# Performance work log

Hardware: AMD Instinct MI355X
Metric: run time of the kernel (lower is better)

## Reference

```python
import jax, jax.numpy as jnp
import numpy as np

HIDDEN = 512
HEADS = 8
HEAD_DIM = HIDDEN // HEADS
MAX_DIST = 10
B, N = 16, 512
EPS = 1e-5


def _layer_norm(x, g, b):
    mu = jnp.mean(x, axis=-1, keepdims=True)
    var = jnp.mean(jnp.square(x - mu), axis=-1, keepdims=True)
    return (x - mu) * jax.lax.rsqrt(var + EPS) * g + b


def setup_inputs() -> dict:
    key = jax.random.key(0)
    ks = jax.random.split(key, 16)
    s = 0.02
    inp = {
        "x": jax.random.normal(ks[0], (B, N, HIDDEN), jnp.float32),
        "distances": jax.random.randint(ks[1], (B, N, N), 0, MAX_DIST, jnp.int32),
        "edge_features": jax.random.normal(ks[2], (B, N, N), jnp.float32),
        "attn_mask": jax.random.randint(ks[3], (B, N), 0, 2).astype(bool),
        "Wq": jax.random.normal(ks[4], (HIDDEN, HIDDEN), jnp.float32) * s,
        "bq": jnp.zeros((HIDDEN,), jnp.float32),
        "Wk": jax.random.normal(ks[5], (HIDDEN, HIDDEN), jnp.float32) * s,
        "bk": jnp.zeros((HIDDEN,), jnp.float32),
        "Wv": jax.random.normal(ks[6], (HIDDEN, HIDDEN), jnp.float32) * s,
        "bv": jnp.zeros((HIDDEN,), jnp.float32),
        "Wo": jax.random.normal(ks[7], (HIDDEN, HIDDEN), jnp.float32) * s,
        "bo": jnp.zeros((HIDDEN,), jnp.float32),
        "spatial_emb": jax.random.normal(ks[8], (MAX_DIST, HEADS), jnp.float32) * s,
        "edge_w": jax.random.normal(ks[9], (HEADS,), jnp.float32) * s,
        "edge_b": jnp.zeros((HEADS,), jnp.float32),
        "ln1_g": jnp.ones((HIDDEN,), jnp.float32),
        "ln1_b": jnp.zeros((HIDDEN,), jnp.float32),
        "ln2_g": jnp.ones((HIDDEN,), jnp.float32),
        "ln2_b": jnp.zeros((HIDDEN,), jnp.float32),
        "W1": jax.random.normal(ks[10], (HIDDEN, 4 * HIDDEN), jnp.float32) * s,
        "b1": jnp.zeros((4 * HIDDEN,), jnp.float32),
        "W2": jax.random.normal(ks[11], (4 * HIDDEN, HIDDEN), jnp.float32) * s,
        "b2": jnp.zeros((HIDDEN,), jnp.float32),
    }
    return inp


def reference(x, distances, edge_features, attn_mask, Wq, bq, Wk, bk, Wv, bv,
              Wo, bo, spatial_emb, edge_w, edge_b, ln1_g, ln1_b, ln2_g, ln2_b,
              W1, b1, W2, b2):
    b, n, _ = x.shape
    q = (x @ Wq + bq).reshape(b, n, HEADS, HEAD_DIM)
    k = (x @ Wk + bk).reshape(b, n, HEADS, HEAD_DIM)
    v = (x @ Wv + bv).reshape(b, n, HEADS, HEAD_DIM)
    # [b, h, i, j] attention scores
    scores = jnp.einsum('bihd,bjhd->bhij', q, k) / np.sqrt(HEAD_DIM).astype(np.float32)
    spatial_bias = spatial_emb[distances]                       # [b, i, j, h]
    edge_bias = edge_features[..., None] * edge_w + edge_b      # [b, i, j, h]
    scores = scores + jnp.transpose(spatial_bias + edge_bias, (0, 3, 1, 2))
    scores = jnp.where(attn_mask[:, None, None, :], -jnp.inf, scores)
    attn = jax.nn.softmax(scores, axis=-1)
    out = jnp.einsum('bhij,bjhd->bihd', attn, v).reshape(b, n, HIDDEN)
    out = out @ Wo + bo
    h = _layer_norm(x + out, ln1_g, ln1_b)
    ffn = jax.nn.relu(h @ W1 + b1) @ W2 + b2
    return _layer_norm(h + ffn, ln2_g, ln2_b)
```

## Files before the change

### kernel.cpp

```cpp
#include <hip/hip_runtime.h>
#include <stdint.h>
#include <stddef.h>

#define SEQ   512
#define HID   512
#define NHEAD 8
#define HD    64
#define NBATCH 16
#define NTOK  8192
#define MAXD  10
#define LOG2E 1.4426950408889634f

typedef __attribute__((ext_vector_type(8))) short short8;
typedef __attribute__((ext_vector_type(4))) float f32x4;

typedef __attribute__((address_space(3))) void        as3_void;
typedef const __attribute__((address_space(1))) void  as1_cvoid;

#define MFMA16(a,b,c) __builtin_amdgcn_mfma_f32_16x16x32_bf16((a),(b),(c),0,0,0)

__device__ __forceinline__ float bf2f(uint16_t u){ return __uint_as_float(((uint32_t)u)<<16); }
__device__ __forceinline__ uint16_t f2bf(float f){
  uint32_t i = __float_as_uint(f);
  return (uint16_t)((i + 0x7fffu + ((i>>16)&1u)) >> 16);
}

enum { EPI_BF16=0, EPI_F32=3, EPI_RELU=4 };

__global__ __launch_bounds__(256) void f2bf_kernel(
    const float* __restrict__ in, uint16_t* __restrict__ out, int n4)
{
  int i = blockIdx.x*256 + threadIdx.x;
  if (i < n4){
    float4 v = *(const float4*)(in + (size_t)i*4);
    *(ushort4*)(out + (size_t)i*4) =
        make_ushort4(f2bf(v.x), f2bf(v.y), f2bf(v.z), f2bf(v.w));
  }
}

__global__ __launch_bounds__(256) void transpose_all(
    const float* __restrict__ Wq, const float* __restrict__ Wk,
    const float* __restrict__ Wv, const float* __restrict__ Wo,
    const float* __restrict__ W1, const float* __restrict__ W2,
    uint16_t* __restrict__ tq, uint16_t* __restrict__ tk,
    uint16_t* __restrict__ tv, uint16_t* __restrict__ to_,
    uint16_t* __restrict__ t1, uint16_t* __restrict__ t2)
{
  __shared__ uint16_t tile[32][33];
  int id = blockIdx.x;
  const float* in; uint16_t* out; int R, C, tx, ty;
  if (id < 1024) {
    int m = id >> 8, loc = id & 255;
    in  = (m==0)?Wq:(m==1)?Wk:(m==2)?Wv:Wo;
    out = (m==0)?tq:(m==1)?tk:(m==2)?tv:to_;
    R = 512; C = 512; ty = loc>>4; tx = loc&15;
  } else if (id < 2048) {
    int loc = id-1024; in=W1; out=t1; R=512; C=2048; ty=loc>>6; tx=loc&63;
  } else {
    int loc = id-2048; in=W2; out=t2; R=2048; C=512; ty=loc>>4; tx=loc&15;
  }
  int bx = tx*32, by = ty*32;
  int lx = threadIdx.x & 31, ly = threadIdx.x >> 5;
  #pragma unroll
  for (int i=ly; i<32; i+=8) tile[i][lx] = f2bf(in[(size_t)(by+i)*C + bx+lx]);
  __syncthreads();
  #pragma unroll
  for (int i=ly; i<32; i+=8) out[(size_t)(bx+i)*R + by+lx] = tile[lx][i];
}

__global__ __launch_bounds__(512) void pack_bias(
    const int*   __restrict__ dist,
    const float* __restrict__ edge,
    const int*   __restrict__ mask,
    uint32_t*    __restrict__ outp)
{
  __shared__ int   dl[16][260];
  __shared__ float el[16][260];
  __shared__ int   ml[512];
  const int b  = blockIdx.y;
  const int it = blockIdx.x;
  const int t  = threadIdx.x;
  ml[t] = mask[b*SEQ + t];

  #pragma unroll
  for (int jh=0; jh<2; ++jh){
    if (jh) __syncthreads();
    {
      const int r  = t >> 5;
      const int c0 = (t & 31) * 8;
      const size_t g = ((size_t)b*SEQ + it*16 + r)*SEQ + jh*256 + c0;
      *(int4*)&dl[r][c0]     = *(const int4*)&dist[g];
      *(int4*)&dl[r][c0+4]   = *(const int4*)&dist[g+4];
      *(float4*)&el[r][c0]   = *(const float4*)&edge[g];
      *(float4*)&el[r][c0+4] = *(const float4*)&edge[g+4];
    }
    __syncthreads();
    {
      const int i   = t & 15;
      const int j0p = (t >> 4) * 8;
      const int jt  = jh*4 + (j0p >> 6);
      const int jn  = (j0p >> 4) & 3;
      const int lg  = (j0p & 15) >> 2;
      uint32_t w[8];
      #pragma unroll
      for (int e=0; e<8; ++e){
        const int jl = j0p + e;
        const int jg = jh*256 + jl;
        const uint32_t d  = (uint32_t)dl[i][jl] & 0xFFu;
        const uint32_t mk = (ml[jg] ? 1u : 0u) << 8;
        w[e] = ((uint32_t)f2bf(el[i][jl]) << 16) | mk | d;
      }
      uint32_t* ob = outp + ((((size_t)b*32 + it)*8 + jt)*64)*16;
      const int lane0 = lg*16 + i, lane1 = (lg+1)*16 + i;
      *(uint4*)&ob[lane0*16 + jn*4] = make_uint4(w[0],w[1],w[2],w[3]);
      *(uint4*)&ob[lane1*16 + jn*4] = make_uint4(w[4],w[5],w[6],w[7]);
    }
  }
}

template<int BM, int BN>
__device__ __forceinline__ void gemm_tile_mainloop(
    const uint16_t* __restrict__ A, const uint16_t* __restrict__ Bt,
    int K, int m0, int n0, uint16_t* lA, uint16_t* lB,
    f32x4 acc[4][(BM==128)?4:((BN==128)?2:1)])
{
  constexpr int NJ  = (BM==128)?4:((BN==128)?2:1);
  constexpr int ARD = BM/32;
  constexpr int BRD = BN/32;
  constexpr bool DB = (BM==64) && (BN==64);
  const int t = threadIdx.x;
  const int w = t>>6, l = t&63;
  const int lg = l>>4, lc = l&15;
  const int wr = (BM==128)?(w>>1):0;
  const int wc = (BM==128)?(w&1):w;
  const int swz = lc & 7;
  const int kSteps = K>>6;

  auto stage = [&](int kt, int buf){
    const int k0 = kt<<6;
    #pragma unroll
    for (int rd=0; rd<ARD; ++rd){
      const int e   = rd*2048 + t*8;
      const int row = e>>6;
      const int col = (((e>>3)&7) ^ (row&7))*8;
      const uint16_t* ga = A + (size_t)(m0+row)*K + (k0+col);
      char* la = (char*)(lA + buf*(BM*64)) + rd*4096 + w*1024;
      __builtin_amdgcn_global_load_lds((as1_cvoid*)ga, (as3_void*)la, 16, 0, 0);
    }
    #pragma unroll
    for (int rd=0; rd<BRD; ++rd){
      const int e   = rd*2048 + t*8;
      const int row = e>>6;
      const int col = (((e>>3)&7) ^ (row&7))*8;
      const uint16_t* gb = Bt + (size_t)(n0+row)*K + (k0+col);
      char* lb = (char*)(lB + buf*(BN*64)) + rd*4096 + w*1024;
      __builtin_amdgcn_global_load_lds((as1_cvoid*)gb, (as3_void*)lb, 16, 0, 0);
    }
  };

  auto compute = [&](const uint16_t* rA, const uint16_t* rB){
    #pragma unroll
    for (int kk=0; kk<2; ++kk){
      const int cc = (kk*4 + lg) ^ swz;
      short8 af[4], bfr[NJ];
      #pragma unroll
      for (int i=0;i<4;i++)
        af[i]  = *(const short8*)&rA[(wr*64 + i*16 + lc)*64 + cc*8];
      #pragma unroll
      for (int j=0;j<NJ;j++)
        bfr[j] = *(const short8*)&rB[(wc*16*NJ + j*16 + lc)*64 + cc*8];
      #pragma unroll
      for (int i=0;i<4;i++)
        #pragma unroll
        for (int j=0;j<NJ;j++)
          acc[i][j] = MFMA16(af[i], bfr[j], acc[i][j]);
    }
  };

  if constexpr (DB){
    stage(0, 0);
    __syncthreads();
    int cur = 0;
    for (int kt=0; kt<kSteps; ++kt){
      if (kt+1 < kSteps) stage(kt+1, cur^1);
      compute(lA + cur*(BM*64), lB + cur*(BN*64));
      __syncthreads();
      cur ^= 1;
    }
  } else {
    for (int kt=0; kt<kSteps; ++kt){
      stage(kt, 0);
      __syncthreads();
      compute(lA, lB);
      __syncthreads();
    }
  }
}

template<int EPI, int BM, int BN>
__global__ __launch_bounds__(256,2) void gemm_bt(
    const uint16_t* __restrict__ A, const uint16_t* __restrict__ Bt,
    const float* __restrict__ bias, void* __restrict__ outp,
    int M, int N, int K)
{
  constexpr int NJ = (BM==128)?4:((BN==128)?2:1);
  constexpr int NB = ((BM==64)&&(BN==64)) ? 2 : 1;
  __shared__ uint16_t lA[NB*BM*64];
  __shared__ uint16_t lB[NB*BN*64];
  f32x4 acc[4][NJ];
  #pragma unroll
  for (int i=0;i<4;i++)
    #pragma unroll
    for (int j=0;j<NJ;j++){ f32x4 z = {0.f,0.f,0.f,0.f}; acc[i][j]=z; }
  const int m0 = blockIdx.x*BM, n0 = blockIdx.y*BN;
  gemm_tile_mainloop<BM,BN>(A, Bt, K, m0, n0, lA, lB, acc);

  const int t=threadIdx.x, w=t>>6, l=t&63, lg=l>>4, lc=l&15;
  const int wr=(BM==128)?(w>>1):0, wc=(BM==128)?(w&1):w;
  #pragma unroll
  for (int j=0;j<NJ;j++){
    const int col = n0 + wc*16*NJ + j*16 + lc;
    const float bs = bias[col];
    #pragma unroll
    for (int i=0;i<4;i++){
      const int rowb = m0 + wr*64 + i*16 + lg*4;
      #pragma unroll
      for (int r=0;r<4;r++){
        float v = acc[i][j][r] + bs;
        if constexpr (EPI==EPI_RELU)   v = fmaxf(v, 0.f);
        if constexpr (EPI==EPI_F32)
          ((float*)outp)[(size_t)(rowb+r)*N + col] = v;
        else
          ((uint16_t*)outp)[(size_t)(rowb+r)*N + col] = f2bf(v);
      }
    }
  }
}

__global__ __launch_bounds__(256,2) void qkv_gemm(
    const uint16_t* __restrict__ x,
    const uint16_t* __restrict__ wtq, const uint16_t* __restrict__ wtk,
    const uint16_t* __restrict__ wtv,
    const float* __restrict__ bq, const float* __restrict__ bk,
    const float* __restrict__ bv,
    uint16_t* __restrict__ qo, uint16_t* __restrict__ kp,
    uint16_t* __restrict__ vp)
{
  __shared__ uint16_t lA[128*64];
  __shared__ uint16_t lB[128*64];
  const int z = blockIdx.z;
  const uint16_t* Bt = (z==0)?wtq:(z==1)?wtk:wtv;
  const float*  bias = (z==0)?bq :(z==1)?bk :bv;
  f32x4 acc[4][4];
  #pragma unroll
  for (int i=0;i<4;i++)
    #pragma unroll
    for (int j=0;j<4;j++){ f32x4 zz = {0.f,0.f,0.f,0.f}; acc[i][j]=zz; }
  const int m0 = blockIdx.x*128, n0 = blockIdx.y*128;
  gemm_tile_mainloop<128,128>(x, Bt, HID, m0, n0, lA, lB, acc);

  const int t=threadIdx.x, w=t>>6, l=t&63, lg=l>>4, lc=l&15, wr=w>>1, wc=w&1;
  if (z==0){
    const float scale = 0.125f * LOG2E;
    #pragma unroll
    for (int j=0;j<4;j++){
      const int col = n0 + wc*64 + j*16 + lc;
      const float bs = bias[col];
      #pragma unroll
      for (int i=0;i<4;i++){
        const int rowb = m0 + wr*64 + i*16 + lg*4;
        #pragma unroll
        for (int r=0;r<4;r++)
          qo[(size_t)(rowb+r)*HID + col] = f2bf((acc[i][j][r] + bs)*scale);
      }
    }
  } else if (z==1){
    #pragma unroll
    for (int j=0;j<4;j++){
      const int col = n0 + wc*64 + j*16 + lc;
      const float bs = bias[col];
      const int h_ = col>>6, cm = col&63, kk = cm>>5, lgk = (cm>>3)&3, e = col&7;
      #pragma unroll
      for (int i=0;i<4;i++){
        const int rowb = m0 + wr*64 + i*16 + lg*4;
        #pragma unroll
        for (int r=0;r<4;r++){
          const int tok = rowb + r;
          const int b_ = tok>>9, tl = tok&511;
          const int jt = tl>>6, jn = (tl>>4)&3, lck = tl&15;
          kp[((((size_t)(b_*8+h_)*8 + jt)*4 + jn)*2 + kk)*512
             + (lgk*16 + lck)*8 + e] = f2bf(acc[i][j][r] + bs);
        }
      }
    }
  } else {
    #pragma unroll
    for (int j=0;j<4;j++){
      const int col = n0 + wc*64 + j*16 + lc;
      const float bs = bias[col];
      const int h_ = col>>6, dn = (col>>4)&3, lcv = col&15;
      #pragma unroll
      for (int i=0;i<4;i++){
        const int rowb = m0 + wr*64 + i*16 + lg*4;
        const int b_ = rowb>>9, tl = rowb&511;
        const int jt = tl>>6, kk = (tl>>5)&1, lgv = (tl>>3)&3, e0 = tl&7;
        *(ushort4*)&vp[((((size_t)(b_*8+h_)*8 + jt)*2 + kk)*4 + dn)*512
                       + (lgv*16 + lcv)*8 + e0] =
            make_ushort4(f2bf(acc[i][j][0]+bs), f2bf(acc[i][j][1]+bs),
                         f2bf(acc[i][j][2]+bs), f2bf(acc[i][j][3]+bs));
      }
    }
  }
}

__global__ __launch_bounds__(512,4) void attn_kernel(
    const uint16_t* __restrict__ q,
    const uint16_t* __restrict__ kp,
    const uint16_t* __restrict__ vp,
    const uint32_t* __restrict__ biasp,
    const float*    __restrict__ semb,
    const float*    __restrict__ ew,
    const float*    __restrict__ eb,
    uint16_t* __restrict__ out)
{
  __shared__ float sp_rep[NHEAD][32][11];
  __shared__ uint16_t plds[NHEAD][2][16*64];
  const int b  = blockIdx.y;
  const int it = blockIdx.x;
  const int i0 = it*16;
  const int t  = threadIdx.x;
  const int h  = t>>6, l = t&63, lg = l>>4, lc = l&15;
  for (int i = t; i < NHEAD*32*MAXD; i += 512){
    const int hh = i / (32*MAXD), rem = i % (32*MAXD);
    const int a = rem / MAXD, d = rem % MAXD;
    sp_rep[hh][a][d] = (semb[d*NHEAD + hh] + eb[hh]) * LOG2E;
  }
  __syncthreads();
  const float ewf = ew[h] * LOG2E;
  const float* spl = &sp_rep[h][l&31][0];
  char* pbase = (char*)&plds[h][0][0];
  const int swz = (lc&7)<<4;

  short8 qf[2];
  #pragma unroll
  for (int kk=0;kk<2;kk++)
    qf[kk] = *(const short8*)&q[(size_t)(b*SEQ + i0 + lc)*HID + h*HD + kk*32 + lg*8];

  const uint4* bp = (const uint4*)(biasp + (((size_t)b*32 + it)*8)*64*16);
  const uint16_t* kpb = kp + (size_t)(b*8+h)*8*4*2*512 + l*8;
  const uint16_t* vpb = vp + (size_t)(b*8+h)*8*2*4*512 + l*8;

  float mrun[2] = {-1e30f, -1e30f};
  float lrun[2] = {0.f, 0.f};
  f32x4 oacc[2][4];
  #pragma unroll
  for (int s=0;s<2;s++)
    #pragma unroll
    for (int dn=0;dn<4;dn++){ f32x4 z={0.f,0.f,0.f,0.f}; oacc[s][dn]=z; }

  #pragma unroll
  for (int p=0; p<4; ++p){
    #pragma unroll
    for (int s=0; s<2; ++s){
      const int jt = s*4 + p;
      uint32_t uw[16];
      {
        const uint4* bq_ = bp + (jt*64 + l)*4;
        *(uint4*)&uw[0]  = bq_[0];
        *(uint4*)&uw[4]  = bq_[1];
        *(uint4*)&uw[8]  = bq_[2];
        *(uint4*)&uw[12] = bq_[3];
      }
      f32x4 st[4];
      #pragma unroll
      for (int jn=0;jn<4;jn++){ f32x4 z={0.f,0.f,0.f,0.f}; st[jn]=z; }
      __builtin_amdgcn_s_setprio(1);
      #pragma unroll
      for (int jn=0;jn<4;jn++){
        #pragma unroll
        for (int kk=0;kk<2;kk++){
          short8 kf = *(const short8*)&kpb[(size_t)((jt*4 + jn)*2 + kk)*512];
          st[jn] = MFMA16(kf, qf[kk], st[jn]);
        }
      }
      __builtin_amdgcn_s_setprio(0);
      float tmax = -1e30f;
      #pragma unroll
      for (int jn=0;jn<4;jn++){
        #pragma unroll
        for (int r=0;r<4;r++){
          const uint32_t u = uw[jn*4+r];
          float sv = st[jn][r] + spl[u & 0xFFu]
                   + bf2f((uint16_t)(u >> 16))*ewf;
          if (u & 0x100u) sv = -1e30f;
          st[jn][r] = sv;
          tmax = fmaxf(tmax, sv);
        }
      }
      {
        float tm = fmaxf(tmax, __shfl_xor(tmax, 16, 64));
        tm = fmaxf(tm, __shfl_xor(tm, 32, 64));
        float mnew = fmaxf(mrun[s], tm);
        mnew = fmaxf(mnew, -1e20f);
        const float c = __builtin_amdgcn_exp2f(mrun[s] - mnew);
        mrun[s] = mnew;
        float lsum = 0.f;
        char* pb = pbase + s*(16*64*2) + lc*128;
        #pragma unroll
        for (int jn=0;jn<4;jn++){
          float p0 = __builtin_amdgcn_exp2f(st[jn][0]-mnew);
          float p1 = __builtin_amdgcn_exp2f(st[jn][1]-mnew);
          float p2 = __builtin_amdgcn_exp2f(st[jn][2]-mnew);
          float p3 = __builtin_amdgcn_exp2f(st[jn][3]-mnew);
          lsum += (p0+p1)+(p2+p3);
          *(ushort4*)(pb + (((jn*16 + lg*4)*2) ^ swz)) =
              make_ushort4(f2bf(p0), f2bf(p1), f2bf(p2), f2bf(p3));
        }
        lrun[s] = lrun[s]*c + lsum;
        #pragma unroll
        for (int r=0;r<4;r++){
          const float cr = __shfl(c, lg*4+r, 64);
          #pragma unroll
          for (int dn=0;dn<4;dn++) oacc[s][dn][r] *= cr;
        }
      }
    }
    #pragma unroll
    for (int s=0; s<2; ++s){
      const int jt = s*4 + p;
      char* pb = pbase + s*(16*64*2) + lc*128;
      __builtin_amdgcn_s_setprio(1);
      #pragma unroll
      for (int kk=0;kk<2;kk++){
        short8 pa = *(const short8*)(pb + (((kk*32 + lg*8)*2) ^ swz));
        #pragma unroll
        for (int dn=0;dn<4;dn++){
          short8 vb = *(const short8*)&vpb[(size_t)((jt*2 + kk)*4 + dn)*512];
          oacc[s][dn] = MFMA16(pa, vb, oacc[s][dn]);
        }
      }
      __builtin_amdgcn_s_setprio(0);
    }
  }
  {
    const float mm = fmaxf(mrun[0], mrun[1]);
    const float c0 = __builtin_amdgcn_exp2f(mrun[0]-mm);
    const float c1 = __builtin_amdgcn_exp2f(mrun[1]-mm);
    float ls = lrun[0]*c0 + lrun[1]*c1;
    ls += __shfl_xor(ls, 16, 64);
    ls += __shfl_xor(ls, 32, 64);
    const float inv = 1.f/ls;
    #pragma unroll
    for (int r=0;r<4;r++){
      const float cr0 = __shfl(c0, lg*4+r, 64);
      const float cr1 = __shfl(c1, lg*4+r, 64);
      const float ir  = __shfl(inv, lg*4+r, 64);
      const size_t orow = ((size_t)b*SEQ + i0 + lg*4 + r)*HID;
      #pragma unroll
      for (int dn=0;dn<4;dn++)
        out[orow + h*HD + dn*16 + lc] =
            f2bf((oacc[0][dn][r]*cr0 + oacc[1][dn][r]*cr1)*ir);
    }
  }
}

__global__ __launch_bounds__(256) void ln_kernel(
    const uint16_t* __restrict__ a, const float* __restrict__ bsrc,
    const float* __restrict__ g, const float* __restrict__ bb,
    float* __restrict__ of, uint16_t* __restrict__ ob)
{
  const int row = blockIdx.x*4 + (threadIdx.x>>6);
  const int l = threadIdx.x & 63;
  const int c0 = l*8;
  const uint16_t* ar = a    + (size_t)row*HID + c0;
  const float*    br = bsrc + (size_t)row*HID + c0;
  short8 av = *(const short8*)ar;
  float4 b0 = *(const float4*)br;
  float4 b1 = *(const float4*)(br+4);
  float u[8];
  u[0]=bf2f((uint16_t)av[0])+b0.x; u[1]=bf2f((uint16_t)av[1])+b0.y;
  u[2]=bf2f((uint16_t)av[2])+b0.z; u[3]=bf2f((uint16_t)av[3])+b0.w;
  u[4]=bf2f((uint16_t)av[4])+b1.x; u[5]=bf2f((uint16_t)av[5])+b1.y;
  u[6]=bf2f((uint16_t)av[6])+b1.z; u[7]=bf2f((uint16_t)av[7])+b1.w;
  float s=0.f, ss=0.f;
  #pragma unroll
  for (int e=0;e<8;e++){ s += u[e]; ss += u[e]*u[e]; }
  #pragma unroll
  for (int off=32; off>=1; off>>=1){
    s  += __shfl_xor(s,  off, 64);
    ss += __shfl_xor(ss, off, 64);
  }
  const float mu  = s*(1.f/512.f);
  const float inv = rsqrtf(ss*(1.f/512.f) - mu*mu + 1e-5f);
  float4 g0 = *(const float4*)(g + c0),  g1 = *(const float4*)(g + c0 + 4);
  float4 q0 = *(const float4*)(bb + c0), q1 = *(const float4*)(bb + c0 + 4);
  float y[8];
  y[0]=(u[0]-mu)*inv*g0.x+q0.x; y[1]=(u[1]-mu)*inv*g0.y+q0.y;
  y[2]=(u[2]-mu)*inv*g0.z+q0.z; y[3]=(u[3]-mu)*inv*g0.w+q0.w;
  y[4]=(u[4]-mu)*inv*g1.x+q1.x; y[5]=(u[5]-mu)*inv*g1.y+q1.y;
  y[6]=(u[6]-mu)*inv*g1.z+q1.z; y[7]=(u[7]-mu)*inv*g1.w+q1.w;
  if (of){
    float* orow = of + (size_t)row*HID + c0;
    *(float4*)orow     = make_float4(y[0],y[1],y[2],y[3]);
    *(float4*)(orow+4) = make_float4(y[4],y[5],y[6],y[7]);
  }
  if (ob){
    uint16_t* brow = ob + (size_t)row*HID + c0;
    *(ushort4*)brow     = make_ushort4(f2bf(y[0]),f2bf(y[1]),f2bf(y[2]),f2bf(y[3]));
    *(ushort4*)(brow+4) = make_ushort4(f2bf(y[4]),f2bf(y[5]),f2bf(y[6]),f2bf(y[7]));
  }
}

extern "C" void kernel_launch(void* const* d_in, const int* in_sizes, int n_in,
                              void* d_out, int out_size, void* d_ws, size_t ws_size,
                              hipStream_t stream)
{
  (void)in_sizes; (void)n_in; (void)out_size; (void)ws_size;
  const float* x    = (const float*)d_in[0];
  const int*   dist = (const int*)  d_in[1];
  const float* edge = (const float*)d_in[2];
  const int*   mask = (const int*)  d_in[3];
  const float* Wq = (const float*)d_in[4];
  const float* bq = (const float*)d_in[5];
  const float* Wk = (const float*)d_in[6];
  const float* bk = (const float*)d_in[7];
  const float* Wv = (const float*)d_in[8];
  const float* bv = (const float*)d_in[9];
  const float* Wo = (const float*)d_in[10];
  const float* bo = (const float*)d_in[11];
  const float* semb = (const float*)d_in[12];
  const float* ew   = (const float*)d_in[13];
  const float* eb   = (const float*)d_in[14];
  const float* ln1g = (const float*)d_in[15];
  const float* ln1b = (const float*)d_in[16];
  const float* ln2g = (const float*)d_in[17];
  const float* ln2b = (const float*)d_in[18];
  const float* W1 = (const float*)d_in[19];
  const float* b1 = (const float*)d_in[20];
  const float* W2 = (const float*)d_in[21];
  const float* b2 = (const float*)d_in[22];

  char* ws = (char*)d_ws;
  uint16_t* xb16  = (uint16_t*)ws;
  uint16_t* qbuf  = xb16  + (size_t)NTOK*HID;
  uint16_t* kpbuf = qbuf  + (size_t)NTOK*HID;
  uint16_t* vpbuf = kpbuf + (size_t)NTOK*HID;
  uint16_t* aobuf = vpbuf + (size_t)NTOK*HID;
  uint16_t* f1buf = qbuf;
  uint32_t* biasp = (uint32_t*)(ws + (size_t)5*NTOK*HID*2);
  uint16_t* tb16  = (uint16_t*)biasp;
  uint16_t* t2b16 = tb16;
  float*    hbuf  = (float*)((char*)biasp + (size_t)NTOK*HID*4);
  uint16_t* hb16  = (uint16_t*)(hbuf + (size_t)NTOK*HID);
  uint16_t* wt    = hb16 + (size_t)NTOK*HID;
  uint16_t* wtq = wt;
  uint16_t* wtk = wtq + 512*512;
  uint16_t* wtv = wtk + 512*512;
  uint16_t* wto = wtv + 512*512;
  uint16_t* wt1 = wto + 512*512;
  uint16_t* wt2 = wt1 + 512*2048;

  pack_bias<<<dim3(32,16), 512, 0, stream>>>(dist, edge, mask, biasp);

  transpose_all<<<3072, 256, 0, stream>>>(Wq,Wk,Wv,Wo,W1,W2, wtq,wtk,wtv,wto,wt1,wt2);

  f2bf_kernel<<<4096, 256, 0, stream>>>(x, xb16, NTOK*HID/4);

  qkv_gemm<<<dim3(64,4,3), 256, 0, stream>>>(xb16, wtq,wtk,wtv, bq,bk,bv,
                                             qbuf, kpbuf, vpbuf);

  attn_kernel<<<dim3(32,16), 512, 0, stream>>>(qbuf, kpbuf, vpbuf, biasp,
                                               semb, ew, eb, aobuf);

  gemm_bt<EPI_BF16,64,64><<<dim3(128,8), 256, 0, stream>>>(aobuf, wto, bo, tb16, NTOK, HID, HID);

  ln_kernel<<<2048, 256, 0, stream>>>(tb16, x, ln1g, ln1b, hbuf, hb16);

  gemm_bt<EPI_RELU,128,128><<<dim3(64,16), 256, 0, stream>>>(hb16, wt1, b1, f1buf, NTOK, 2048, HID);

  gemm_bt<EPI_BF16,64,64><<<dim3(128,8), 256, 0, stream>>>(f1buf, wt2, b2, t2b16, NTOK, HID, 2048);

  ln_kernel<<<2048, 256, 0, stream>>>(t2b16, hbuf, ln2g, ln2b, (float*)d_out, nullptr);
}
```

Before: 160.4 us.

## Double-buffer all GEMM tiles, merge prep kernels, truncate softmax probabilities

```diff
diff --git a/kernel.cpp b/kernel.cpp
--- a/kernel.cpp
+++ b/kernel.cpp
@@ -24,21 +24,14 @@
   uint32_t i = __float_as_uint(f);
   return (uint16_t)((i + 0x7fffu + ((i>>16)&1u)) >> 16);
 }
+__device__ __forceinline__ uint16_t f2bf_rtz(float f){
+  return (uint16_t)(__float_as_uint(f) >> 16);
+}
 
 enum { EPI_BF16=0, EPI_F32=3, EPI_RELU=4 };
 
-__global__ __launch_bounds__(256) void f2bf_kernel(
-    const float* __restrict__ in, uint16_t* __restrict__ out, int n4)
-{
-  int i = blockIdx.x*256 + threadIdx.x;
-  if (i < n4){
-    float4 v = *(const float4*)(in + (size_t)i*4);
-    *(ushort4*)(out + (size_t)i*4) =
-        make_ushort4(f2bf(v.x), f2bf(v.y), f2bf(v.z), f2bf(v.w));
-  }
-}
-
-__global__ __launch_bounds__(256) void transpose_all(
+__global__ __launch_bounds__(256) void prep_kernel(
+    const float* __restrict__ x, uint16_t* __restrict__ xb,
     const float* __restrict__ Wq, const float* __restrict__ Wk,
     const float* __restrict__ Wv, const float* __restrict__ Wo,
     const float* __restrict__ W1, const float* __restrict__ W2,
@@ -46,8 +39,17 @@
     uint16_t* __restrict__ tv, uint16_t* __restrict__ to_,
     uint16_t* __restrict__ t1, uint16_t* __restrict__ t2)
 {
+  int id = blockIdx.x;
+  if (id >= 3072){
+    int i = (id-3072)*256 + threadIdx.x;
+    if (i < NTOK*HID/4){
+      float4 v = *(const float4*)(x + (size_t)i*4);
+      *(ushort4*)(xb + (size_t)i*4) =
+          make_ushort4(f2bf(v.x), f2bf(v.y), f2bf(v.z), f2bf(v.w));
+    }
+    return;
+  }
   __shared__ uint16_t tile[32][33];
-  int id = blockIdx.x;
   const float* in; uint16_t* out; int R, C, tx, ty;
   if (id < 1024) {
     int m = id >> 8, loc = id & 255;
@@ -127,7 +129,6 @@
   constexpr int NJ  = (BM==128)?4:((BN==128)?2:1);
   constexpr int ARD = BM/32;
   constexpr int BRD = BN/32;
-  constexpr bool DB = (BM==64) && (BN==64);
   const int t = threadIdx.x;
   const int w = t>>6, l = t&63;
   const int lg = l>>4, lc = l&15;
@@ -177,23 +178,14 @@
     }
   };
 
-  if constexpr (DB){
-    stage(0, 0);
+  stage(0, 0);
+  __syncthreads();
+  int cur = 0;
+  for (int kt=0; kt<kSteps; ++kt){
+    if (kt+1 < kSteps) stage(kt+1, cur^1);
+    compute(lA + cur*(BM*64), lB + cur*(BN*64));
     __syncthreads();
-    int cur = 0;
-    for (int kt=0; kt<kSteps; ++kt){
-      if (kt+1 < kSteps) stage(kt+1, cur^1);
-      compute(lA + cur*(BM*64), lB + cur*(BN*64));
-      __syncthreads();
-      cur ^= 1;
-    }
-  } else {
-    for (int kt=0; kt<kSteps; ++kt){
-      stage(kt, 0);
-      __syncthreads();
-      compute(lA, lB);
-      __syncthreads();
-    }
+    cur ^= 1;
   }
 }
 
@@ -204,9 +196,8 @@
     int M, int N, int K)
 {
   constexpr int NJ = (BM==128)?4:((BN==128)?2:1);
-  constexpr int NB = ((BM==64)&&(BN==64)) ? 2 : 1;
-  __shared__ uint16_t lA[NB*BM*64];
-  __shared__ uint16_t lB[NB*BN*64];
+  __shared__ uint16_t lA[2*BM*64];
+  __shared__ uint16_t lB[2*BN*64];
   f32x4 acc[4][NJ];
   #pragma unroll
   for (int i=0;i<4;i++)
@@ -246,8 +237,8 @@
     uint16_t* __restrict__ qo, uint16_t* __restrict__ kp,
     uint16_t* __restrict__ vp)
 {
-  __shared__ uint16_t lA[128*64];
-  __shared__ uint16_t lB[128*64];
+  __shared__ uint16_t lA[2*128*64];
+  __shared__ uint16_t lB[2*128*64];
   const int z = blockIdx.z;
   const uint16_t* Bt = (z==0)?wtq:(z==1)?wtk:wtv;
   const float*  bias = (z==0)?bq :(z==1)?bk :bv;
@@ -323,21 +314,21 @@
     const float*    __restrict__ eb,
     uint16_t* __restrict__ out)
 {
-  __shared__ float sp_rep[NHEAD][32][11];
+  __shared__ float sp_rep[NHEAD][64][11];
   __shared__ uint16_t plds[NHEAD][2][16*64];
   const int b  = blockIdx.y;
   const int it = blockIdx.x;
   const int i0 = it*16;
   const int t  = threadIdx.x;
   const int h  = t>>6, l = t&63, lg = l>>4, lc = l&15;
-  for (int i = t; i < NHEAD*32*MAXD; i += 512){
-    const int hh = i / (32*MAXD), rem = i % (32*MAXD);
+  for (int i = t; i < NHEAD*64*MAXD; i += 512){
+    const int hh = i / (64*MAXD), rem = i % (64*MAXD);
     const int a = rem / MAXD, d = rem % MAXD;
     sp_rep[hh][a][d] = (semb[d*NHEAD + hh] + eb[hh]) * LOG2E;
   }
   __syncthreads();
   const float ewf = ew[h] * LOG2E;
-  const float* spl = &sp_rep[h][l&31][0];
+  const float* spl = &sp_rep[h][l][0];
   char* pbase = (char*)&plds[h][0][0];
   const int swz = (lc&7)<<4;
 
@@ -414,7 +405,8 @@
           float p3 = __builtin_amdgcn_exp2f(st[jn][3]-mnew);
           lsum += (p0+p1)+(p2+p3);
           *(ushort4*)(pb + (((jn*16 + lg*4)*2) ^ swz)) =
-              make_ushort4(f2bf(p0), f2bf(p1), f2bf(p2), f2bf(p3));
+              make_ushort4(f2bf_rtz(p0), f2bf_rtz(p1),
+                           f2bf_rtz(p2), f2bf_rtz(p3));
         }
         lrun[s] = lrun[s]*c + lsum;
         #pragma unroll
@@ -562,9 +554,8 @@
 
   pack_bias<<<dim3(32,16), 512, 0, stream>>>(dist, edge, mask, biasp);
 
-  transpose_all<<<3072, 256, 0, stream>>>(Wq,Wk,Wv,Wo,W1,W2, wtq,wtk,wtv,wto,wt1,wt2);
-
-  f2bf_kernel<<<4096, 256, 0, stream>>>(x, xb16, NTOK*HID/4);
+  prep_kernel<<<7168, 256, 0, stream>>>(x, xb16, Wq,Wk,Wv,Wo,W1,W2,
+                                        wtq,wtk,wtv,wto,wt1,wt2);
 
   qkv_gemm<<<dim3(64,4,3), 256, 0, stream>>>(xb16, wtq,wtk,wtv, bq,bk,bv,
                                              qbuf, kpbuf, vpbuf);
```

After: 159.3 us. Within noise of the previous version (-0.7%).
